# Kernel tuning notes

Hardware: AMD Instinct MI355X
Metric: run time of the kernel (lower is better)

## Reference

```python
import jax, jax.numpy as jnp
import numpy as np


def setup_inputs() -> dict:
    key = jax.random.key(0)
    ks = jax.random.split(key, 8)
    B, T, U = 4, 256, 128
    E, D, J, V = 512, 640, 640, 1024
    enc = jax.random.normal(ks[0], (B, T, E), dtype=jnp.float32)
    dec = jax.random.normal(ks[1], (B, U, D), dtype=jnp.float32)
    # Linear params (kaiming-uniform-ish scale is irrelevant for correctness; use scaled normals)
    W_enc = jax.random.normal(ks[2], (E, J), dtype=jnp.float32) / np.sqrt(E)
    b_enc = jax.random.normal(ks[3], (J,), dtype=jnp.float32) * 0.01
    W_dec = jax.random.normal(ks[4], (D, J), dtype=jnp.float32) / np.sqrt(D)
    b_dec = jax.random.normal(ks[5], (J,), dtype=jnp.float32) * 0.01
    W_joint = jax.random.normal(ks[6], (J, V), dtype=jnp.float32) / np.sqrt(J)
    b_joint = jax.random.normal(ks[7], (V,), dtype=jnp.float32) * 0.01
    return {
        "encoder_outputs": enc,
        "decoder_outputs": dec,
        "W_enc": W_enc, "b_enc": b_enc,
        "W_dec": W_dec, "b_dec": b_dec,
        "W_joint": W_joint, "b_joint": b_joint,
    }


def reference(encoder_outputs, decoder_outputs, W_enc, b_enc, W_dec, b_dec, W_joint, b_joint):
    # enc_proj: (B,T,J); dec_proj: (B,U,J)
    enc_proj = jnp.einsum('bte,ej->btj', encoder_outputs, W_enc) + b_enc
    dec_proj = jnp.einsum('bud,dj->buj', decoder_outputs, W_dec) + b_dec
    # broadcast add -> (B,T,U,J), tanh, then project to vocab
    joint = jnp.tanh(enc_proj[:, :, None, :] + dec_proj[:, None, :, :])
    logits = jnp.einsum('btuj,jv->btuv', joint, W_joint) + b_joint
    return logits
```

## Files before the change

### kernel.cpp

```cpp
#include <hip/hip_runtime.h>
#include <stdint.h>

typedef float  f4     __attribute__((ext_vector_type(4)));
typedef float  f32x4  __attribute__((ext_vector_type(4)));
typedef __bf16 bf16x8 __attribute__((ext_vector_type(8)));

#define AS_GLOBAL __attribute__((address_space(1)))
#define AS_LDS    __attribute__((address_space(3)))

constexpr int Bdim = 4, T = 256, U = 128, E = 512, Dd = 640, J = 640, V = 1024;

__device__ __forceinline__ void lds_load16(void* lds, const void* g) {
  __builtin_amdgcn_global_load_lds(
      (const AS_GLOBAL uint32_t*)(uintptr_t)g,
      (AS_LDS uint32_t*)(uint32_t)(uintptr_t)lds, 16, 0, 0);
}

__device__ __forceinline__ float fast_tanh(float x) {
  float e = __builtin_amdgcn_exp2f(x * 2.88539008177f);
  return 1.0f - 2.0f * __builtin_amdgcn_rcpf(e + 1.0f);
}

__global__ __launch_bounds__(256) void proj_kernel(
    const float* __restrict__ X, const float* __restrict__ W,
    const float* __restrict__ bias, float* __restrict__ out, int K) {
  const int tid = threadIdx.x;
  const int jt  = tid & 127;
  const int h   = tid >> 7;
  const int r0  = blockIdx.x * 4;
  __shared__ float sX[4 * 640];
  __shared__ float sAcc[4 * 5 * 128];

  for (int idx = tid * 4; idx < 4 * K; idx += 1024)
    *(f4*)&sX[idx] = *(const f4*)&X[(size_t)r0 * K + idx];
  __syncthreads();

  float acc[4][5] = {};
  const int e0 = h * (K >> 1), e1 = e0 + (K >> 1);
  for (int e = e0; e < e1; e += 4) {
    f4 xr[4];
#pragma unroll
    for (int r = 0; r < 4; ++r) xr[r] = *(const f4*)&sX[r * K + e];
#pragma unroll
    for (int i = 0; i < 4; ++i) {
#pragma unroll
      for (int q = 0; q < 5; ++q) {
        float w = W[(size_t)(e + i) * J + q * 128 + jt];
#pragma unroll
        for (int r = 0; r < 4; ++r) acc[r][q] = fmaf(xr[r][i], w, acc[r][q]);
      }
    }
  }
  if (h == 1) {
#pragma unroll
    for (int r = 0; r < 4; ++r)
#pragma unroll
      for (int q = 0; q < 5; ++q) sAcc[(r * 5 + q) * 128 + jt] = acc[r][q];
  }
  __syncthreads();
  if (h == 0) {
#pragma unroll
    for (int r = 0; r < 4; ++r)
#pragma unroll
      for (int q = 0; q < 5; ++q) {
        float v = acc[r][q] + sAcc[(r * 5 + q) * 128 + jt] + bias[q * 128 + jt];
        out[(size_t)(r0 + r) * J + q * 128 + jt] = v;
      }
  }
}

__global__ __launch_bounds__(256) void transpose_wj(const float* __restrict__ W,
                                                    __bf16* __restrict__ Wt) {
  __shared__ float t[32][33];
  const int v0 = blockIdx.x * 32, j0 = blockIdx.y * 32;
  const int c = threadIdx.x & 31, r = threadIdx.x >> 5;
#pragma unroll
  for (int rr = 0; rr < 4; ++rr)
    t[r + rr * 8][c] = W[(size_t)(j0 + r + rr * 8) * V + v0 + c];
  __syncthreads();
#pragma unroll
  for (int rr = 0; rr < 4; ++rr)
    Wt[(size_t)(v0 + r + rr * 8) * J + j0 + c] = (__bf16)t[c][r + rr * 8];
}

constexpr int JBM = 64, JBN = 256, JBK = 64;

__global__ __launch_bounds__(256, 3) void joint_kernel(
    const float* __restrict__ ep, const float* __restrict__ dp,
    const __bf16* __restrict__ Wt, const float* __restrict__ bj,
    float* __restrict__ out) {
  const int mblk = blockIdx.y;
  const int bt   = mblk >> 1;
  const int u0   = (mblk & 1) * JBM;
  const int b    = bt >> 8;
  const int v0   = blockIdx.x * JBN;
  const int tid  = threadIdx.x;
  const int wv   = tid >> 6, lane = tid & 63;
  const int lrow = lane & 15, lq = lane >> 4;

  __shared__ __align__(16) __bf16 As[JBM * JBK];
  __shared__ __align__(16) __bf16 Bs[JBN * JBK];

  const float* epr = ep + (size_t)bt * J;
  const float* dpr = dp + ((size_t)b * U + u0) * J;

  f32x4 acc[4][4];
#pragma unroll
  for (int fn = 0; fn < 4; ++fn) {
    const float bv = bj[v0 + wv * 64 + fn * 16 + lrow];
#pragma unroll
    for (int fm = 0; fm < 4; ++fm) acc[fm][fn] = (f32x4){bv, bv, bv, bv};
  }

  const int ar = tid >> 3;
  const int as = tid & 7;
  const int aw = (as ^ (ar & 7));

  for (int k0 = 0; k0 < J; k0 += JBK) {
    {
      const int ssrc = as ^ (ar & 7);
      const __bf16* src0 = Wt + (size_t)(v0 + ar) * J + k0 + ssrc * 8;
#pragma unroll
      for (int i = 0; i < 8; ++i)
        lds_load16((char*)Bs + (size_t)(i * 256 + tid) * 16,
                   src0 + (size_t)i * 32 * J);
    }
#pragma unroll
    for (int hh = 0; hh < 2; ++hh) {
      const int r = ar + hh * 32;
      const float* ds = dpr + (size_t)r * J + k0 + as * 8;
      const float* es = epr + k0 + as * 8;
      f4 d0 = *(const f4*)ds, d1 = *(const f4*)(ds + 4);
      f4 e0 = *(const f4*)es, e1 = *(const f4*)(es + 4);
      bf16x8 av;
#pragma unroll
      for (int i = 0; i < 4; ++i) av[i]     = (__bf16)fast_tanh(d0[i] + e0[i]);
#pragma unroll
      for (int i = 0; i < 4; ++i) av[i + 4] = (__bf16)fast_tanh(d1[i] + e1[i]);
      *(bf16x8*)((char*)As + r * 128 + aw * 16) = av;
    }
    __syncthreads();

#pragma unroll
    for (int hh = 0; hh < 2; ++hh) {
      bf16x8 af[4], bfr[4];
#pragma unroll
      for (int f = 0; f < 4; ++f) {
        const int rm = f * 16 + lrow;
        af[f] = *(const bf16x8*)((char*)As + rm * 128 +
                                 (((lq + 4 * hh) ^ (rm & 7)) * 16));
        const int rn = wv * 64 + f * 16 + lrow;
        bfr[f] = *(const bf16x8*)((char*)Bs + rn * 128 +
                                  (((lq + 4 * hh) ^ (rn & 7)) * 16));
      }
#pragma unroll
      for (int fm = 0; fm < 4; ++fm)
#pragma unroll
        for (int fn = 0; fn < 4; ++fn)
          acc[fm][fn] = __builtin_amdgcn_mfma_f32_16x16x32_bf16(
              af[fm], bfr[fn], acc[fm][fn], 0, 0, 0);
    }
    __syncthreads();
  }

  const size_t rowbase = (size_t)bt * U + u0;
#pragma unroll
  for (int fn = 0; fn < 4; ++fn) {
    const int col = v0 + wv * 64 + fn * 16 + lrow;
#pragma unroll
    for (int fm = 0; fm < 4; ++fm) {
      const int u = fm * 16 + lq * 4;
#pragma unroll
      for (int i = 0; i < 4; ++i)
        out[(rowbase + u + i) * (size_t)V + col] = acc[fm][fn][i];
    }
  }
}

extern "C" void kernel_launch(void* const* d_in, const int* in_sizes, int n_in,
                              void* d_out, int out_size, void* d_ws, size_t ws_size,
                              hipStream_t stream) {
  (void)in_sizes; (void)n_in; (void)out_size; (void)ws_size;
  const float* enc    = (const float*)d_in[0];
  const float* dec    = (const float*)d_in[1];
  const float* W_enc  = (const float*)d_in[2];
  const float* b_enc  = (const float*)d_in[3];
  const float* W_dec  = (const float*)d_in[4];
  const float* b_dec  = (const float*)d_in[5];
  const float* W_jnt  = (const float*)d_in[6];
  const float* b_jnt  = (const float*)d_in[7];
  float* out = (float*)d_out;

  float*  ep = (float*)d_ws;
  float*  dp = ep + (size_t)Bdim * T * J;
  __bf16* Wt = (__bf16*)(dp + (size_t)Bdim * U * J);

  proj_kernel<<<dim3(Bdim * T / 4), 256, 0, stream>>>(enc, W_enc, b_enc, ep, E);
  proj_kernel<<<dim3(Bdim * U / 4), 256, 0, stream>>>(dec, W_dec, b_dec, dp, Dd);
  transpose_wj<<<dim3(V / 32, J / 32), 256, 0, stream>>>(W_jnt, Wt);
  joint_kernel<<<dim3(V / JBN, Bdim * T * U / JBM), 256, 0, stream>>>(ep, dp, Wt, b_jnt, out);
}
```

Baseline: 851.8 us.

## Double-buffer joint kernel LDS tiles with halved K step and prefetch

Splits the joint GEMM K loop into 32-wide steps with ping-pong LDS buffers for the tanh activations and the transposed weights. The next tile's weight loads and activation reads are issued before the current MFMAs, and the tanh for the next tile is computed after them, so only one barrier remains per step. It also drops the XOR swizzle in favour of a plain row layout and raises wave priority around the MFMA block. Risks are LDS bank conflicts from the unswizzled 64-byte rows, twice as many loop iterations, and more LDS per block at three blocks per CU.

```diff
diff --git a/kernel.cpp b/kernel.cpp
--- a/kernel.cpp
+++ b/kernel.cpp
@@ -83,7 +83,7 @@
     Wt[(size_t)(v0 + r + rr * 8) * J + j0 + c] = (__bf16)t[c][r + rr * 8];
 }
 
-constexpr int JBM = 64, JBN = 256, JBK = 64;
+constexpr int JBM = 64, JBN = 256, JBK = 32;
 
 __global__ __launch_bounds__(256, 3) void joint_kernel(
     const float* __restrict__ ep, const float* __restrict__ dp,
@@ -98,8 +98,8 @@
   const int wv   = tid >> 6, lane = tid & 63;
   const int lrow = lane & 15, lq = lane >> 4;
 
-  __shared__ __align__(16) __bf16 As[JBM * JBK];
-  __shared__ __align__(16) __bf16 Bs[JBN * JBK];
+  __shared__ __align__(16) __bf16 As[2][JBM * JBK];
+  __shared__ __align__(16) __bf16 Bs[2][JBN * JBK];
 
   const float* epr = ep + (size_t)bt * J;
   const float* dpr = dp + ((size_t)b * U + u0) * J;
@@ -112,55 +112,88 @@
     for (int fm = 0; fm < 4; ++fm) acc[fm][fn] = (f32x4){bv, bv, bv, bv};
   }
 
-  const int ar = tid >> 3;
-  const int as = tid & 7;
-  const int aw = (as ^ (ar & 7));
-
-  for (int k0 = 0; k0 < J; k0 += JBK) {
+  const int nr   = tid >> 2;
+  const int slot = tid & 3;
+  const int ar   = tid >> 2;
+  const int ak   = (tid & 3) * 8;
+
+  const __bf16* bsrc = Wt + (size_t)(v0 + nr) * J + slot * 8;
+
+#pragma unroll
+  for (int i = 0; i < 4; ++i)
+    lds_load16((char*)Bs[0] + (size_t)(i * 256 + tid) * 16,
+               bsrc + (size_t)i * 64 * J);
+  {
+    const float* ds = dpr + (size_t)ar * J + ak;
+    const float* es = epr + ak;
+    f4 d0 = *(const f4*)ds, d1 = *(const f4*)(ds + 4);
+    f4 e0 = *(const f4*)es, e1 = *(const f4*)(es + 4);
+    bf16x8 av;
+#pragma unroll
+    for (int i = 0; i < 4; ++i) av[i]     = (__bf16)fast_tanh(d0[i] + e0[i]);
+#pragma unroll
+    for (int i = 0; i < 4; ++i) av[i + 4] = (__bf16)fast_tanh(d1[i] + e1[i]);
+    *(bf16x8*)&As[0][ar * JBK + ak] = av;
+  }
+  __syncthreads();
+
+  int cur = 0;
+  for (int t = 0; t < 19; ++t) {
+    const int kn  = (t + 1) * JBK;
+    const int nxt = cur ^ 1;
+
+#pragma unroll
+    for (int i = 0; i < 4; ++i)
+      lds_load16((char*)Bs[nxt] + (size_t)(i * 256 + tid) * 16,
+                 bsrc + (size_t)kn + (size_t)i * 64 * J);
+
+    const float* ds = dpr + (size_t)ar * J + kn + ak;
+    const float* es = epr + kn + ak;
+    f4 d0 = *(const f4*)ds, d1 = *(const f4*)(ds + 4);
+    f4 e0 = *(const f4*)es, e1 = *(const f4*)(es + 4);
+
+    bf16x8 af[4], bfr[4];
+#pragma unroll
+    for (int f = 0; f < 4; ++f) {
+      af[f]  = *(const bf16x8*)&As[cur][(f * 16 + lrow) * JBK + lq * 8];
+      bfr[f] = *(const bf16x8*)&Bs[cur][(wv * 64 + f * 16 + lrow) * JBK + lq * 8];
+    }
+
+    __builtin_amdgcn_s_setprio(1);
+#pragma unroll
+    for (int fm = 0; fm < 4; ++fm)
+#pragma unroll
+      for (int fn = 0; fn < 4; ++fn)
+        acc[fm][fn] = __builtin_amdgcn_mfma_f32_16x16x32_bf16(
+            af[fm], bfr[fn], acc[fm][fn], 0, 0, 0);
+    __builtin_amdgcn_s_setprio(0);
+
     {
-      const int ssrc = as ^ (ar & 7);
-      const __bf16* src0 = Wt + (size_t)(v0 + ar) * J + k0 + ssrc * 8;
-#pragma unroll
-      for (int i = 0; i < 8; ++i)
-        lds_load16((char*)Bs + (size_t)(i * 256 + tid) * 16,
-                   src0 + (size_t)i * 32 * J);
-    }
-#pragma unroll
-    for (int hh = 0; hh < 2; ++hh) {
-      const int r = ar + hh * 32;
-      const float* ds = dpr + (size_t)r * J + k0 + as * 8;
-      const float* es = epr + k0 + as * 8;
-      f4 d0 = *(const f4*)ds, d1 = *(const f4*)(ds + 4);
-      f4 e0 = *(const f4*)es, e1 = *(const f4*)(es + 4);
       bf16x8 av;
 #pragma unroll
       for (int i = 0; i < 4; ++i) av[i]     = (__bf16)fast_tanh(d0[i] + e0[i]);
 #pragma unroll
       for (int i = 0; i < 4; ++i) av[i + 4] = (__bf16)fast_tanh(d1[i] + e1[i]);
-      *(bf16x8*)((char*)As + r * 128 + aw * 16) = av;
-    }
+      *(bf16x8*)&As[nxt][ar * JBK + ak] = av;
+    }
+
     __syncthreads();
-
-#pragma unroll
-    for (int hh = 0; hh < 2; ++hh) {
-      bf16x8 af[4], bfr[4];
-#pragma unroll
-      for (int f = 0; f < 4; ++f) {
-        const int rm = f * 16 + lrow;
-        af[f] = *(const bf16x8*)((char*)As + rm * 128 +
-                                 (((lq + 4 * hh) ^ (rm & 7)) * 16));
-        const int rn = wv * 64 + f * 16 + lrow;
-        bfr[f] = *(const bf16x8*)((char*)Bs + rn * 128 +
-                                  (((lq + 4 * hh) ^ (rn & 7)) * 16));
-      }
-#pragma unroll
-      for (int fm = 0; fm < 4; ++fm)
-#pragma unroll
-        for (int fn = 0; fn < 4; ++fn)
-          acc[fm][fn] = __builtin_amdgcn_mfma_f32_16x16x32_bf16(
-              af[fm], bfr[fn], acc[fm][fn], 0, 0, 0);
-    }
-    __syncthreads();
+    cur = nxt;
+  }
+
+  {
+    bf16x8 af[4], bfr[4];
+#pragma unroll
+    for (int f = 0; f < 4; ++f) {
+      af[f]  = *(const bf16x8*)&As[cur][(f * 16 + lrow) * JBK + lq * 8];
+      bfr[f] = *(const bf16x8*)&Bs[cur][(wv * 64 + f * 16 + lrow) * JBK + lq * 8];
+    }
+#pragma unroll
+    for (int fm = 0; fm < 4; ++fm)
+#pragma unroll
+      for (int fn = 0; fn < 4; ++fn)
+        acc[fm][fn] = __builtin_amdgcn_mfma_f32_16x16x32_bf16(
+            af[fm], bfr[fn], acc[fm][fn], 0, 0, 0);
   }
 
   const size_t rowbase = (size_t)bt * U + u0;
```

Measured after the change: 886.8 us. +4.1%, slower.
